# Kernel optimization log

Measured on AMD Instinct MI355X. Metric: run time of the kernel, lower is better.

Reference implementation:

```python
import jax, jax.numpy as jnp
import numpy as np

N_HEADS = 16
N_KV_HEADS = 4
WINDOW = 128
THETA = 10000.0


def _rope_cos_sin(T, half):
    inv = 1.0 / (THETA ** (jnp.arange(half, dtype=jnp.float32) / half))
    f = jnp.arange(T, dtype=jnp.float32)[:, None] * inv[None, :]  # (T, half)
    return jnp.cos(f), jnp.sin(f)


def _apply_rope(x, cos, sin):
    # x: (B, H, T, hd); interleaved (real, imag) pairs like torch view_as_complex
    xr, xi = x[..., 0::2], x[..., 1::2]
    out_r = xr * cos - xi * sin
    out_i = xr * sin + xi * cos
    return jnp.stack([out_r, out_i], axis=-1).reshape(x.shape)


def setup_inputs() -> dict:
    key = jax.random.key(0)
    ks = jax.random.split(key, 6)
    B, T, C = 1, 4096, 2048
    kvC = (C // N_HEADS) * N_KV_HEADS
    return {
        "x": jax.random.normal(ks[0], (B, T, C), dtype=jnp.float32),
        "wq": jax.random.normal(ks[1], (C, C), dtype=jnp.float32) * 0.02,
        "wk": jax.random.normal(ks[2], (C, kvC), dtype=jnp.float32) * 0.02,
        "wv": jax.random.normal(ks[3], (C, kvC), dtype=jnp.float32) * 0.02,
        "wo": jax.random.normal(ks[4], (C, C), dtype=jnp.float32) * 0.02,
        "sink": jnp.zeros((1, N_HEADS, 1, 1), dtype=jnp.float32),
    }


def reference(x, wq, wk, wv, wo, sink):
    B, T, C = x.shape
    hd = C // N_HEADS
    n_rep = N_HEADS // N_KV_HEADS

    q = (x @ wq).reshape(B, T, N_HEADS, hd).transpose(0, 2, 1, 3)    # (B,H,T,hd)
    k = (x @ wk).reshape(B, T, N_KV_HEADS, hd).transpose(0, 2, 1, 3)  # (B,Hkv,T,hd)
    v = (x @ wv).reshape(B, T, N_KV_HEADS, hd).transpose(0, 2, 1, 3)

    cos, sin = _rope_cos_sin(T, hd // 2)  # (T, hd/2), broadcasts over (B,H,T,hd/2)
    q = _apply_rope(q, cos, sin)
    k = _apply_rope(k, cos, sin)

    # GQA head expansion (repeat_interleave over head dim)
    k = jnp.repeat(k, n_rep, axis=1)
    v = jnp.repeat(v, n_rep, axis=1)

    att = jnp.einsum("bhqd,bhkd->bhqk", q, k) * (hd ** -0.5) + sink

    # symmetric sliding-window band: |i - j| <= window//2
    idx = jnp.arange(T)
    band = jnp.abs(idx[:, None] - idx[None, :]) <= (WINDOW // 2)
    att = jnp.where(band[None, None, :, :], att, -jnp.inf)

    att = jax.nn.softmax(att, axis=-1)
    # torch code replaces NaN rows (fully-masked) with uniform; band always has diag so no-op
    att = jnp.where(jnp.isnan(att), 1.0 / T, att)

    out = jnp.einsum("bhqk,bhkd->bqhd", att, v).reshape(B, T, C)
    return out @ wo
```

## Files before the change

kernel.cpp:

```cpp
#include <hip/hip_runtime.h>
#include <stdint.h>

#define T_SEQ 4096
#define C_DIM 2048
#define HD 128

typedef unsigned short ushort_t;
typedef __attribute__((ext_vector_type(8))) short shortx8;
typedef __attribute__((ext_vector_type(4))) float floatx4;
typedef __attribute__((ext_vector_type(8))) unsigned short u16x8;
typedef __attribute__((ext_vector_type(4))) unsigned short u16x4;

__device__ __forceinline__ ushort_t f2bf(float f) {
  union { float f; uint32_t u; } v; v.f = f;
  v.u += 0x7fffu + ((v.u >> 16) & 1u);
  return (ushort_t)(v.u >> 16);
}
__device__ __forceinline__ void load_lds16(const ushort_t* g, ushort_t* l) {
  __builtin_amdgcn_global_load_lds(
      (const __attribute__((address_space(1))) unsigned int*)g,
      (__attribute__((address_space(3))) unsigned int*)l, 16, 0, 0);
}

__global__ __launch_bounds__(256) void prep_kernel(
    const float* __restrict__ wq, const float* __restrict__ wk,
    const float* __restrict__ wv, const float* __restrict__ wo,
    const float* __restrict__ x,
    ushort_t* __restrict__ BtAll, ushort_t* __restrict__ woT,
    ushort_t* __restrict__ xb) {
  const int bid = blockIdx.x;
  const int tid = threadIdx.x;
  if (bid >= 2560) {
    int i = (bid - 2560) * 256 + tid;
    float4 v = ((const float4*)x)[i];
    u16x4 o; o[0] = f2bf(v.x); o[1] = f2bf(v.y); o[2] = f2bf(v.z); o[3] = f2bf(v.w);
    ((u16x4*)xb)[i] = o;
    return;
  }
  const float* src; ushort_t* dst; int C, bx, by;
  if (bid < 1024) { src = wq; dst = BtAll; C = 2048; bx = bid & 31; by = bid >> 5; }
  else if (bid < 1280) { int b = bid - 1024; src = wk; dst = BtAll + (size_t)2048 * 2048; C = 512; bx = b & 7; by = b >> 3; }
  else if (bid < 1536) { int b = bid - 1280; src = wv; dst = BtAll + (size_t)2560 * 2048; C = 512; bx = b & 7; by = b >> 3; }
  else { int b = bid - 1536; src = wo; dst = woT; C = 2048; bx = b & 31; by = b >> 5; }
  const int R = 2048;

  __shared__ float tile[64][65];
  const int c0 = bx * 64, r0 = by * 64;
  for (int i = tid; i < 1024; i += 256) {
    int r = i >> 4, cc = (i & 15) * 4;
    float4 v = *(const float4*)&src[(size_t)(r0 + r) * C + c0 + cc];
    tile[r][cc] = v.x; tile[r][cc + 1] = v.y; tile[r][cc + 2] = v.z; tile[r][cc + 3] = v.w;
  }
  __syncthreads();
  for (int i = tid; i < 512; i += 256) {
    int oc = i >> 3;
    int g = (i & 7) * 8;
    u16x8 o;
    for (int j = 0; j < 8; ++j) o[j] = f2bf(tile[g + j][oc]);
    *(u16x8*)&dst[(size_t)(c0 + oc) * R + r0 + g] = o;
  }
}

struct GemmAcc { floatx4 a[4][4]; };

__device__ __forceinline__ void gemm_core_bk64(
    const ushort_t* __restrict__ A, const ushort_t* __restrict__ Bt,
    ushort_t* As, ushort_t* Bs, GemmAcc& acc,
    int m0, int n0, int K, int tid, int lane, int wave, int quad, int l16,
    int wm, int wn) {
  const int nk = K >> 6;
  for (int kk = 0; kk < nk; ++kk) {
    const int k0 = kk << 6;
    for (int r = 0; r < 4; ++r) {
      int e = r * 256 + tid;
      int row = e >> 3;
      int p = e & 7;
      int g = (p - row) & 7;
      const ushort_t* ga = A + (size_t)(m0 + row) * K + k0 + g * 8;
      const ushort_t* gb = Bt + (size_t)(n0 + row) * K + k0 + g * 8;
      ushort_t* la = As + (size_t)(r * 256 + (tid & 192)) * 8;
      ushort_t* lb = Bs + (size_t)(r * 256 + (tid & 192)) * 8;
      load_lds16(ga, la);
      load_lds16(gb, lb);
    }
    __syncthreads();
    for (int ks = 0; ks < 2; ++ks) {
      shortx8 af[4], bfr[4];
      for (int i = 0; i < 4; ++i) {
        int ar = wm + i * 16 + l16;
        af[i] = *(const shortx8*)(As + ar * 64 + (((ks << 2) + quad + ar) & 7) * 8);
        int br = wn + i * 16 + l16;
        bfr[i] = *(const shortx8*)(Bs + br * 64 + (((ks << 2) + quad + br) & 7) * 8);
      }
      for (int i = 0; i < 4; ++i)
        for (int j = 0; j < 4; ++j)
          acc.a[i][j] = __builtin_amdgcn_mfma_f32_16x16x32_bf16(af[i], bfr[j], acc.a[i][j], 0, 0, 0);
    }
    __syncthreads();
  }
}

__global__ __launch_bounds__(256, 3) void gemm_bf16(
    const ushort_t* __restrict__ A, const ushort_t* __restrict__ Bt,
    float* __restrict__ C, int M, int N, int K) {
  __shared__ __align__(16) ushort_t As[128 * 64];
  __shared__ __align__(16) ushort_t Bs[128 * 64];
  const int tid = threadIdx.x;
  const int lane = tid & 63;
  const int wave = tid >> 6;
  const int quad = lane >> 4;
  const int l16 = lane & 15;
  const int m0 = blockIdx.y * 128;
  const int n0 = blockIdx.x * 128;
  const int wm = (wave & 1) * 64;
  const int wn = (wave >> 1) * 64;

  GemmAcc acc = {};
  gemm_core_bk64(A, Bt, As, Bs, acc, m0, n0, K, tid, lane, wave, quad, l16, wm, wn);

  for (int i = 0; i < 4; ++i)
    for (int j = 0; j < 4; ++j) {
      int col = n0 + wn + j * 16 + l16;
      int rbase = m0 + wm + i * 16 + quad * 4;
      for (int r = 0; r < 4; ++r)
        C[(size_t)(rbase + r) * N + col] = acc.a[i][j][r];
    }
}

#define BARF() do { __builtin_amdgcn_s_barrier(); asm volatile("" ::: "memory"); } while (0)
#define LGKM0() asm volatile("s_waitcnt lgkmcnt(0)" ::: "memory")

__global__ __launch_bounds__(512, 2) void gemm_qkv256(
    const ushort_t* __restrict__ A, const ushort_t* __restrict__ Bt,
    ushort_t* __restrict__ qbb, ushort_t* __restrict__ kbb,
    ushort_t* __restrict__ vtb) {
  __shared__ __align__(16) ushort_t SA[2][16384];
  __shared__ __align__(16) ushort_t SB[2][16384];
  const int tid = threadIdx.x;
  const int lane = tid & 63;
  const int w = tid >> 6;
  const int l16 = lane & 15;
  const int quad = lane >> 4;
  const int wm = (w >> 2) * 128;
  const int wn = (w & 3) * 64;
  const int aq = wm + (w & 3) * 16;
  const int bq = wn + (w >> 2) * 16;
  const int gl8 = lane >> 3;
  const int gch = ((lane & 7) - gl8) & 7;

  const int bid = blockIdx.x;
  const int swz = (bid & 7) * 24 + (bid >> 3);
  const int n0 = (swz % 12) * 256;
  const int m0 = (swz / 12) * 256;

  const int off0 = l16 * 64 + ((quad + l16) & 7) * 8;
  const int off1 = l16 * 64 + ((4 + quad + l16) & 7) * 8;

  floatx4 acc[8][4] = {};
  shortx8 af0[4], af1[4], bf0[2], bf1[2];

  auto issue2 = [&](const ushort_t* __restrict__ G, int gRow, ushort_t* L, int r0, int k0) {
#pragma unroll
    for (int u = 0; u < 2; ++u) {
      const ushort_t* src = G + (size_t)(gRow + r0 + u * 8 + gl8) * 2048 + k0 + gch * 8;
      load_lds16(src, L + (r0 + u * 8) * 64);
    }
  };

#define LOAD_A(base, Sb)                                          \
  _Pragma("unroll")                                               \
  for (int i2 = 0; i2 < 4; ++i2) {                                \
    const int rb = (wm + ((base) + i2) * 16) * 64;                \
    af0[i2] = *(const shortx8*)&(Sb)[rb + off0];                  \
    af1[i2] = *(const shortx8*)&(Sb)[rb + off1];                  \
  }
#define LOAD_B(jb, Sb)                                            \
  _Pragma("unroll")                                               \
  for (int j2 = 0; j2 < 2; ++j2) {                                \
    const int rb = (wn + ((jb) + j2) * 16) * 64;                  \
    bf0[j2] = *(const shortx8*)&(Sb)[rb + off0];                  \
    bf1[j2] = *(const shortx8*)&(Sb)[rb + off1];                  \
  }
#define MFMA16(ih, jh)                                            \
  __builtin_amdgcn_s_setprio(1);                                  \
  _Pragma("unroll")                                               \
  for (int i2 = 0; i2 < 4; ++i2)                                  \
    _Pragma("unroll")                                             \
    for (int j2 = 0; j2 < 2; ++j2) {                              \
      acc[(ih)*4+i2][(jh)*2+j2] = __builtin_amdgcn_mfma_f32_16x16x32_bf16( \
          af0[i2], bf0[j2], acc[(ih)*4+i2][(jh)*2+j2], 0, 0, 0);  \
      acc[(ih)*4+i2][(jh)*2+j2] = __builtin_amdgcn_mfma_f32_16x16x32_bf16( \
          af1[i2], bf1[j2], acc[(ih)*4+i2][(jh)*2+j2], 0, 0, 0);  \
    }                                                             \
  __builtin_amdgcn_s_setprio(0);

  issue2(A, m0, SA[0], aq, 0);        issue2(A, m0, SA[0], aq + 64, 0);
  issue2(Bt, n0, SB[0], bq, 0);       issue2(Bt, n0, SB[0], bq + 32, 0);
  issue2(A, m0, SA[1], aq + 64, 64);  issue2(Bt, n0, SB[1], bq + 32, 64);
  asm volatile("s_waitcnt vmcnt(4)" ::: "memory");
  BARF();

  for (int t2 = 0; t2 < 16; ++t2) {
#pragma unroll
    for (int half = 0; half < 2; ++half) {
      const int t = t2 * 2 + half;
      ushort_t* SAb = SA[half];
      ushort_t* SBb = SB[half];
      ushort_t* SAo = SA[half ^ 1];
      ushort_t* SBo = SB[half ^ 1];

      LOAD_A(0, SAb);
      LOAD_B(0, SBb);
      if (t + 1 < 32) issue2(A, m0, SAo, aq, (t + 1) * 64);
      BARF(); LGKM0();
      MFMA16(0, 0);
      BARF();

      LOAD_B(2, SBb);
      if (t + 1 < 32) issue2(Bt, n0, SBo, bq, (t + 1) * 64);
      BARF(); LGKM0();
      MFMA16(0, 1);
      BARF();

      LOAD_A(4, SAb);
      if (t + 2 < 32) issue2(Bt, n0, SBb, bq + 32, (t + 2) * 64);
      BARF(); LGKM0();
      MFMA16(1, 1);
      BARF();

      LOAD_B(0, SBb);
      if (t + 2 < 32) issue2(A, m0, SAb, aq + 64, (t + 2) * 64);
      BARF(); LGKM0();
      MFMA16(1, 0);
      if (t < 30)       { asm volatile("s_waitcnt vmcnt(4)" ::: "memory"); }
      else if (t == 30) { asm volatile("s_waitcnt vmcnt(0)" ::: "memory"); }
      BARF();
    }
  }

  asm volatile("s_waitcnt vmcnt(0) lgkmcnt(0)" ::: "memory");
  BARF();

  if (n0 < 2560) {
    const bool isq = (n0 < 2048);
    const int par = l16 & 1;
#pragma unroll
    for (int j = 0; j < 4; ++j) {
      int col = n0 + wn + j * 16 + l16;
      int irot = (col & 127) >> 1;
      float inv = __expf(-0.14391157f * (float)irot);
#pragma unroll
      for (int i = 0; i < 8; ++i) {
        int t0r = m0 + wm + i * 16 + quad * 4;
#pragma unroll
        for (int r = 0; r < 4; ++r) {
          float val = acc[i][j][r];
          float other = __shfl_xor(val, 1, 64);
          float sn, cs;
          __sincosf((float)(t0r + r) * inv, &sn, &cs);
          float outv = par ? (other * sn + val * cs) : (val * cs - other * sn);
          if (isq) qbb[(size_t)(t0r + r) * 2048 + col] = f2bf(outv);
          else     kbb[(size_t)(t0r + r) * 512 + (col - 2048)] = f2bf(outv);
        }
      }
    }
  } else {
#pragma unroll
    for (int j = 0; j < 4; ++j) {
      int dim = n0 + wn + j * 16 + l16 - 2560;
#pragma unroll
      for (int i = 0; i < 8; ++i) {
        int t0r = m0 + wm + i * 16 + quad * 4;
        u16x4 o;
#pragma unroll
        for (int r = 0; r < 4; ++r) o[r] = f2bf(acc[i][j][r]);
        *(u16x4*)&vtb[(size_t)dim * T_SEQ + t0r] = o;
      }
    }
  }
#undef LOAD_A
#undef LOAD_B
#undef MFMA16
}

#define LSTR 168
__global__ __launch_bounds__(256, 2) void attn_kernel(
    const ushort_t* __restrict__ qbb, const ushort_t* __restrict__ kbb,
    const ushort_t* __restrict__ vtb, ushort_t* __restrict__ ao) {
  __shared__ __align__(16) ushort_t QP[64 * LSTR];
  __shared__ __align__(16) ushort_t KV[160 * LSTR];

  const int tid = threadIdx.x;
  const int lane = tid & 63;
  const int wave = tid >> 6;
  const int l16 = lane & 15;
  const int quad = lane >> 4;
  const int h0 = blockIdx.x * 2;
  const int kvh = h0 >> 2;
  const int t0 = blockIdx.y * 32;
  const int kstart = t0 - 64;
  const int hsel = wave & 1;
  const int qh = wave >> 1;
  const float scale = 0.08838834764831845f;

  for (int c = tid; c < 1024; c += 256) {
    int row = c >> 4, c8 = c & 15;
    int h = h0 + (row >> 5);
    int q = t0 + (row & 31);
    u16x8 v = *(const u16x8*)&qbb[(size_t)q * C_DIM + h * HD + c8 * 8];
    *(u16x8*)&QP[row * LSTR + c8 * 8] = v;
  }
  for (int c = tid; c < 2560; c += 256) {
    int row = c >> 4, c8 = c & 15;
    int t = kstart + row;
    u16x8 v;
    if (t >= 0 && t < T_SEQ) {
      v = *(const u16x8*)&kbb[(size_t)t * 512 + kvh * HD + c8 * 8];
    } else {
      for (int z = 0; z < 8; ++z) v[z] = 0;
    }
    *(u16x8*)&KV[row * LSTR + c8 * 8] = v;
  }
  __syncthreads();

  floatx4 acc[10] = {};
  const int arow = hsel * 32 + qh * 16 + l16;
  for (int ks = 0; ks < 4; ++ks) {
    shortx8 af = *(const shortx8*)&QP[arow * LSTR + ks * 32 + quad * 8];
    for (int kt = 0; kt < 10; ++kt) {
      shortx8 bf = *(const shortx8*)&KV[(kt * 16 + l16) * LSTR + ks * 32 + quad * 8];
      acc[kt] = __builtin_amdgcn_mfma_f32_16x16x32_bf16(af, bf, acc[kt], 0, 0, 0);
    }
  }

  float mrow[4] = {-3e38f, -3e38f, -3e38f, -3e38f};
  for (int kt = 0; kt < 10; ++kt) {
    int col = kt * 16 + l16;
    int kg = kstart + col;
    for (int r = 0; r < 4; ++r) {
      int row = qh * 16 + quad * 4 + r;
      bool valid = (kg >= 0) && (kg < T_SEQ) && (col >= row) && (col <= row + 128);
      float s = valid ? acc[kt][r] * scale : -3e38f;
      acc[kt][r] = s;
      mrow[r] = fmaxf(mrow[r], s);
    }
  }
  for (int off = 1; off < 16; off <<= 1)
    for (int r = 0; r < 4; ++r)
      mrow[r] = fmaxf(mrow[r], __shfl_xor(mrow[r], off, 64));
  float rl[4];
  for (int r = 0; r < 4; ++r) {
    float s = 0.f;
    for (int kt = 0; kt < 10; ++kt) {
      float p = __expf(acc[kt][r] - mrow[r]);
      acc[kt][r] = p;
      s += p;
    }
    rl[r] = s;
  }
  for (int off = 1; off < 16; off <<= 1)
    for (int r = 0; r < 4; ++r) rl[r] += __shfl_xor(rl[r], off, 64);
  for (int r = 0; r < 4; ++r) rl[r] = 1.0f / rl[r];

  __syncthreads();

  for (int kt = 0; kt < 10; ++kt) {
    int col = kt * 16 + l16;
    for (int r = 0; r < 4; ++r) {
      int row = hsel * 32 + qh * 16 + quad * 4 + r;
      QP[row * LSTR + col] = f2bf(acc[kt][r] * rl[r]);
    }
  }
  for (int c = tid; c < 2560; c += 256) {
    int dim = c / 20, c8 = c % 20;
    int k0 = kstart + c8 * 8;
    const ushort_t* g = &vtb[(size_t)(kvh * HD + dim) * T_SEQ];
    u16x8 v;
    if (k0 >= 0 && k0 + 7 < T_SEQ) {
      v = *(const u16x8*)&g[k0];
    } else {
      for (int z = 0; z < 8; ++z) {
        int kk = k0 + z;
        v[z] = (kk >= 0 && kk < T_SEQ) ? g[kk] : (ushort_t)0;
      }
    }
    *(u16x8*)&KV[dim * LSTR + c8 * 8] = v;
  }
  __syncthreads();

  floatx4 oacc[8] = {};
  const int prow = hsel * 32 + qh * 16 + l16;
  for (int ks = 0; ks < 5; ++ks) {
    shortx8 pf = *(const shortx8*)&QP[prow * LSTR + ks * 32 + quad * 8];
    for (int dt = 0; dt < 8; ++dt) {
      shortx8 vf = *(const shortx8*)&KV[(dt * 16 + l16) * LSTR + ks * 32 + quad * 8];
      oacc[dt] = __builtin_amdgcn_mfma_f32_16x16x32_bf16(pf, vf, oacc[dt], 0, 0, 0);
    }
  }

  const int h = h0 + hsel;
  for (int r = 0; r < 4; ++r) {
    int row = t0 + qh * 16 + quad * 4 + r;
    for (int dt = 0; dt < 8; ++dt) {
      int dim = dt * 16 + l16;
      ao[(size_t)row * C_DIM + h * HD + dim] = f2bf(oacc[dt][r]);
    }
  }
}

extern "C" void kernel_launch(void* const* d_in, const int* in_sizes, int n_in,
                              void* d_out, int out_size, void* d_ws, size_t ws_size,
                              hipStream_t stream) {
  const float* x  = (const float*)d_in[0];
  const float* wq = (const float*)d_in[1];
  const float* wk = (const float*)d_in[2];
  const float* wv = (const float*)d_in[3];
  const float* wo = (const float*)d_in[4];
  float* out = (float*)d_out;

  char* ws = (char*)d_ws;
  ushort_t* BtAll = (ushort_t*)(ws);
  ushort_t* woT   = (ushort_t*)(ws + 12582912);
  ushort_t* xb    = (ushort_t*)(ws + 20971520);
  ushort_t* qbb   = (ushort_t*)(ws + 37748736);
  ushort_t* kbb   = (ushort_t*)(ws + 54525952);
  ushort_t* vtb   = (ushort_t*)(ws + 58720256);
  ushort_t* ao    = (ushort_t*)(ws + 62914560);

  prep_kernel<<<10752, 256, 0, stream>>>(wq, wk, wv, wo, x, BtAll, woT, xb);

  gemm_qkv256<<<192, 512, 0, stream>>>(xb, BtAll, qbb, kbb, vtb);

  attn_kernel<<<dim3(8, 128), 256, 0, stream>>>(qbb, kbb, vtb, ao);

  gemm_bf16<<<dim3(16, 32), 256, 0, stream>>>(ao, woT, out, 4096, 2048, 2048);
}
```

Baseline: 258.6 us.

## Share K/V tiles across all four query heads and prefetch GEMM fragments

The attention kernel now uses one 512-thread block per KV head, handling all four query heads that share it. Each K/V window is loaded from global memory once instead of twice, at the cost of one block per CU and more LDS (roughly 97 KB per block). In the QKV GEMM, A and B LDS fragments go into separate named register sets and are loaded one stage earlier. The explicit lgkmcnt(0) waits are removed, so LDS reads can overlap the MFMAs. This raises register pressure and relies on compiler-inserted waits and barriers to keep LDS reuse safe.

```diff
diff --git a/kernel.cpp b/kernel.cpp
--- a/kernel.cpp
+++ b/kernel.cpp
@@ -128,7 +128,6 @@
 }
 
 #define BARF() do { __builtin_amdgcn_s_barrier(); asm volatile("" ::: "memory"); } while (0)
-#define LGKM0() asm volatile("s_waitcnt lgkmcnt(0)" ::: "memory")
 
 __global__ __launch_bounds__(512, 2) void gemm_qkv256(
     const ushort_t* __restrict__ A, const ushort_t* __restrict__ Bt,
@@ -157,7 +156,8 @@
   const int off1 = l16 * 64 + ((4 + quad + l16) & 7) * 8;
 
   floatx4 acc[8][4] = {};
-  shortx8 af0[4], af1[4], bf0[2], bf1[2];
+  shortx8 a0k0[4], a0k1[4], a1k0[4], a1k1[4];
+  shortx8 b0k0[2], b0k1[2], b1k0[2], b1k1[2];
 
   auto issue2 = [&](const ushort_t* __restrict__ G, int gRow, ushort_t* L, int r0, int k0) {
 #pragma unroll
@@ -167,30 +167,30 @@
     }
   };
 
-#define LOAD_A(base, Sb)                                          \
+#define LOAD_A(base, Sb, D0, D1)                                  \
   _Pragma("unroll")                                               \
   for (int i2 = 0; i2 < 4; ++i2) {                                \
     const int rb = (wm + ((base) + i2) * 16) * 64;                \
-    af0[i2] = *(const shortx8*)&(Sb)[rb + off0];                  \
-    af1[i2] = *(const shortx8*)&(Sb)[rb + off1];                  \
-  }
-#define LOAD_B(jb, Sb)                                            \
+    D0[i2] = *(const shortx8*)&(Sb)[rb + off0];                   \
+    D1[i2] = *(const shortx8*)&(Sb)[rb + off1];                   \
+  }
+#define LOAD_B(jb, Sb, D0, D1)                                    \
   _Pragma("unroll")                                               \
   for (int j2 = 0; j2 < 2; ++j2) {                                \
     const int rb = (wn + ((jb) + j2) * 16) * 64;                  \
-    bf0[j2] = *(const shortx8*)&(Sb)[rb + off0];                  \
-    bf1[j2] = *(const shortx8*)&(Sb)[rb + off1];                  \
-  }
-#define MFMA16(ih, jh)                                            \
+    D0[j2] = *(const shortx8*)&(Sb)[rb + off0];                   \
+    D1[j2] = *(const shortx8*)&(Sb)[rb + off1];                   \
+  }
+#define MFMA16(ih, jh, A0, A1, B0, B1)                            \
   __builtin_amdgcn_s_setprio(1);                                  \
   _Pragma("unroll")                                               \
   for (int i2 = 0; i2 < 4; ++i2)                                  \
     _Pragma("unroll")                                             \
     for (int j2 = 0; j2 < 2; ++j2) {                              \
       acc[(ih)*4+i2][(jh)*2+j2] = __builtin_amdgcn_mfma_f32_16x16x32_bf16( \
-          af0[i2], bf0[j2], acc[(ih)*4+i2][(jh)*2+j2], 0, 0, 0);  \
+          A0[i2], B0[j2], acc[(ih)*4+i2][(jh)*2+j2], 0, 0, 0);    \
       acc[(ih)*4+i2][(jh)*2+j2] = __builtin_amdgcn_mfma_f32_16x16x32_bf16( \
-          af1[i2], bf1[j2], acc[(ih)*4+i2][(jh)*2+j2], 0, 0, 0);  \
+          A1[i2], B1[j2], acc[(ih)*4+i2][(jh)*2+j2], 0, 0, 0);    \
     }                                                             \
   __builtin_amdgcn_s_setprio(0);
 
@@ -209,29 +209,28 @@
       ushort_t* SAo = SA[half ^ 1];
       ushort_t* SBo = SB[half ^ 1];
 
-      LOAD_A(0, SAb);
-      LOAD_B(0, SBb);
+      LOAD_A(0, SAb, a0k0, a0k1);
+      LOAD_B(0, SBb, b0k0, b0k1);
+      LOAD_B(2, SBb, b1k0, b1k1);
       if (t + 1 < 32) issue2(A, m0, SAo, aq, (t + 1) * 64);
-      BARF(); LGKM0();
-      MFMA16(0, 0);
-      BARF();
-
-      LOAD_B(2, SBb);
+      BARF();
+      MFMA16(0, 0, a0k0, a0k1, b0k0, b0k1);
+      BARF();
+
+      LOAD_A(4, SAb, a1k0, a1k1);
       if (t + 1 < 32) issue2(Bt, n0, SBo, bq, (t + 1) * 64);
-      BARF(); LGKM0();
-      MFMA16(0, 1);
-      BARF();
-
-      LOAD_A(4, SAb);
+      BARF();
+      MFMA16(0, 1, a0k0, a0k1, b1k0, b1k1);
+      BARF();
+
       if (t + 2 < 32) issue2(Bt, n0, SBb, bq + 32, (t + 2) * 64);
-      BARF(); LGKM0();
-      MFMA16(1, 1);
-      BARF();
-
-      LOAD_B(0, SBb);
+      BARF();
+      MFMA16(1, 1, a1k0, a1k1, b1k0, b1k1);
+      BARF();
+
       if (t + 2 < 32) issue2(A, m0, SAb, aq + 64, (t + 2) * 64);
-      BARF(); LGKM0();
-      MFMA16(1, 0);
+      BARF();
+      MFMA16(1, 0, a1k0, a1k1, b0k0, b0k1);
       if (t < 30)       { asm volatile("s_waitcnt vmcnt(4)" ::: "memory"); }
       else if (t == 30) { asm volatile("s_waitcnt vmcnt(0)" ::: "memory"); }
       BARF();
@@ -284,10 +283,10 @@
 }
 
 #define LSTR 168
-__global__ __launch_bounds__(256, 2) void attn_kernel(
+__global__ __launch_bounds__(512, 1) void attn_kernel(
     const ushort_t* __restrict__ qbb, const ushort_t* __restrict__ kbb,
     const ushort_t* __restrict__ vtb, ushort_t* __restrict__ ao) {
-  __shared__ __align__(16) ushort_t QP[64 * LSTR];
+  __shared__ __align__(16) ushort_t QP[128 * LSTR];
   __shared__ __align__(16) ushort_t KV[160 * LSTR];
 
   const int tid = threadIdx.x;
@@ -295,22 +294,22 @@
   const int wave = tid >> 6;
   const int l16 = lane & 15;
   const int quad = lane >> 4;
-  const int h0 = blockIdx.x * 2;
-  const int kvh = h0 >> 2;
+  const int kvh = blockIdx.x;
+  const int h0 = kvh * 4;
   const int t0 = blockIdx.y * 32;
   const int kstart = t0 - 64;
-  const int hsel = wave & 1;
-  const int qh = wave >> 1;
+  const int hsel = wave & 3;
+  const int qh = wave >> 2;
   const float scale = 0.08838834764831845f;
 
-  for (int c = tid; c < 1024; c += 256) {
+  for (int c = tid; c < 2048; c += 512) {
     int row = c >> 4, c8 = c & 15;
     int h = h0 + (row >> 5);
     int q = t0 + (row & 31);
     u16x8 v = *(const u16x8*)&qbb[(size_t)q * C_DIM + h * HD + c8 * 8];
     *(u16x8*)&QP[row * LSTR + c8 * 8] = v;
   }
-  for (int c = tid; c < 2560; c += 256) {
+  for (int c = tid; c < 2560; c += 512) {
     int row = c >> 4, c8 = c & 15;
     int t = kstart + row;
     u16x8 v;
@@ -371,7 +370,7 @@
       QP[row * LSTR + col] = f2bf(acc[kt][r] * rl[r]);
     }
   }
-  for (int c = tid; c < 2560; c += 256) {
+  for (int c = tid; c < 2560; c += 512) {
     int dim = c / 20, c8 = c % 20;
     int k0 = kstart + c8 * 8;
     const ushort_t* g = &vtb[(size_t)(kvh * HD + dim) * T_SEQ];
@@ -431,7 +430,7 @@
 
   gemm_qkv256<<<192, 512, 0, stream>>>(xb, BtAll, qbb, kbb, vtb);
 
-  attn_kernel<<<dim3(8, 128), 256, 0, stream>>>(qbb, kbb, vtb, ao);
+  attn_kernel<<<dim3(4, 128), 512, 0, stream>>>(qbb, kbb, vtb, ao);
 
   gemm_bf16<<<dim3(16, 32), 256, 0, stream>>>(ao, woT, out, 4096, 2048, 2048);
 }
```

New measurement: 256.6 us. About the same (-0.7%).
